# Optimization experiments

Measured on AMD Instinct MI355X. Metric: run time of the kernel, lower is better.

## Reference

```python
import jax, jax.numpy as jnp
import numpy as np

N, E = 50000, 600000
D_IN, D_H, D_OUT = 512, 128, 1
BN_EPS = 1e-5


def setup_inputs() -> dict:
    key = jax.random.key(0)
    ks = jax.random.split(key, 16)
    s = 0.05
    inp = {
        "feature": jax.random.normal(ks[0], (N, D_IN), dtype=jnp.float32),
        "edge_index": jax.random.randint(ks[1], (2, E), 0, N, dtype=jnp.int32),
        "head_W": jax.random.normal(ks[2], (D_IN, D_H), dtype=jnp.float32) * s,
        "head_b": jnp.zeros((D_H,), dtype=jnp.float32),
        "gin_W1": jax.random.normal(ks[3], (D_H, D_H), dtype=jnp.float32) * s,
        "gin_b1": jnp.zeros((D_H,), dtype=jnp.float32),
        "lin_W1": jax.random.normal(ks[4], (D_H, D_H), dtype=jnp.float32) * s,
        "lin_b1": jnp.zeros((D_H,), dtype=jnp.float32),
        "gin_W2": jax.random.normal(ks[5], (D_H, D_H), dtype=jnp.float32) * s,
        "gin_b2": jnp.zeros((D_H,), dtype=jnp.float32),
        "lin_W2": jax.random.normal(ks[6], (D_H, D_H), dtype=jnp.float32) * s,
        "lin_b2": jnp.zeros((D_H,), dtype=jnp.float32),
        "tail_W": jax.random.normal(ks[7], (D_H, D_OUT), dtype=jnp.float32) * s,
        "tail_b": jnp.zeros((D_OUT,), dtype=jnp.float32),
        "bn_gamma": jnp.ones((D_OUT,), dtype=jnp.float32),
        "bn_beta": jnp.zeros((D_OUT,), dtype=jnp.float32),
    }
    return inp


def _gin_layer(x, src, dst, gin_W, gin_b, lin_W, lin_b):
    # PyG GINConv, eps=0: nn((1+eps)*x + sum_{j in N(i)} x_j)
    agg = jax.ops.segment_sum(x[src], dst, num_segments=N)  # [N, D_H]
    h = jax.nn.relu((x + agg) @ gin_W + gin_b)              # GIN MLP (dropout p=0)
    return h @ lin_W + lin_b                                # plain post-linear


def reference(feature, edge_index, head_W, head_b,
              gin_W1, gin_b1, lin_W1, lin_b1,
              gin_W2, gin_b2, lin_W2, lin_b2,
              tail_W, tail_b, bn_gamma, bn_beta):
    src, dst = edge_index[0], edge_index[1]
    x = jax.nn.relu(feature @ head_W + head_b)              # head block (dropout p=0)
    x = _gin_layer(x, src, dst, gin_W1, gin_b1, lin_W1, lin_b1)
    x = _gin_layer(x, src, dst, gin_W2, gin_b2, lin_W2, lin_b2)
    z = x @ tail_W + tail_b                                 # [N, 1]
    # BatchNorm1d in training mode: biased batch stats over the node dim
    mu = jnp.mean(z, axis=0, keepdims=True)
    var = jnp.mean((z - mu) ** 2, axis=0, keepdims=True)
    return (z - mu) * jax.lax.rsqrt(var + BN_EPS) * bn_gamma + bn_beta
```

## Files before the change

### kernel.cpp

```cpp
#include <hip/hip_runtime.h>

#define N_NODES 50000
#define N_EDGES 600000
#define DH 128
#define BN_EPS 1e-5f
#define SCAN_BLOCKS ((N_NODES + 255) / 256)

typedef __attribute__((ext_vector_type(8))) short bf16x8;
typedef __attribute__((ext_vector_type(4))) float f32x4;

__device__ inline unsigned short f2bf(float x) {
  unsigned u = __float_as_uint(x);
  return (unsigned short)((u + 0x7FFFu + ((u >> 16) & 1u)) >> 16);
}
__device__ inline float bf2f(unsigned short h) {
  return __uint_as_float(((unsigned)h) << 16);
}

__device__ inline void gl_lds16(const unsigned short* g, unsigned short* l) {
  __builtin_amdgcn_global_load_lds(
      (const __attribute__((address_space(1))) unsigned int*)g,
      (__attribute__((address_space(3))) unsigned int*)l, 16, 0, 0);
}

__global__ __launch_bounds__(256) void convert_W5_count(
    const float* __restrict__ hW, const float* __restrict__ g1,
    const float* __restrict__ l1, const float* __restrict__ g2,
    const float* __restrict__ l2,
    unsigned short* __restrict__ hH, unsigned short* __restrict__ hL,
    unsigned short* __restrict__ g1H, unsigned short* __restrict__ g1L,
    unsigned short* __restrict__ l1H, unsigned short* __restrict__ l1L,
    unsigned short* __restrict__ g2H, unsigned short* __restrict__ g2L,
    unsigned short* __restrict__ l2H, unsigned short* __restrict__ l2L,
    const int* __restrict__ eidx, int* __restrict__ cnt) {
  int b = blockIdx.x;
  if (b >= 512) {
    int e = (b - 512) * 256 + threadIdx.x;
    if (e < N_EDGES) atomicAdd(&cnt[eidx[N_EDGES + e]], 1);
    return;
  }
  const float* W;
  unsigned short *hi, *lo;
  int idx;
  if (b < 256) {
    W = hW; hi = hH; lo = hL;
    idx = b * 256 + threadIdx.x;
  } else {
    int w = (b - 256) >> 6;
    idx = ((b - 256) & 63) * 256 + threadIdx.x;
    W = (w == 0) ? g1 : (w == 1) ? l1 : (w == 2) ? g2 : l2;
    hi = (w == 0) ? g1H : (w == 1) ? l1H : (w == 2) ? g2H : l2H;
    lo = (w == 0) ? g1L : (w == 1) ? l1L : (w == 2) ? g2L : l2L;
  }
  int k = idx >> 7;
  int n = idx & 127;
  float x = W[idx];
  unsigned short h = f2bf(x);
  unsigned short l = f2bf(x - bf2f(h));
  int kstep = k >> 5;
  int ctile = ((n >> 6) << 2) | (n & 3);
  int cs = (n >> 2) & 15;
  int lane = ((k >> 3) & 3) * 16 + cs;
  int j = k & 7;
  size_t off = ((size_t)(kstep * 8 + ctile) * 64 + lane) * 8 + j;
  hi[off] = h;
  lo[off] = l;
}

__global__ __launch_bounds__(256) void gemm_head(const float* __restrict__ A,
                                                 const unsigned short* __restrict__ Bh,
                                                 const unsigned short* __restrict__ Bl,
                                                 const float* __restrict__ bias,
                                                 float* __restrict__ C,
                                                 unsigned short* __restrict__ xb_out,
                                                 int M) {
  constexpr int K = 512;
  constexpr int KSTEPS = K / 32;
  constexpr int ASTR = 40;
  __shared__ __align__(16) unsigned short Ah[64 * ASTR];
  __shared__ __align__(16) unsigned short Bhs[4096];
  __shared__ __align__(16) unsigned short Bls[4096];

  const int tid = threadIdx.x;
  const int wave = tid >> 6;
  const int lane = tid & 63;
  const int m0 = blockIdx.x * 64;

  const int s_row = tid >> 2;
  const int s_grp = tid & 3;
  const int g_row = m0 + s_row;
  const int g_rowc = (g_row < M) ? g_row : (M - 1);
  const float* af = A + (size_t)g_rowc * K + s_grp * 8;

  const int rgrp = wave & 1;
  const int ch = wave >> 1;

  f32x4 acc[2][4];
#pragma unroll
  for (int r = 0; r < 2; ++r)
#pragma unroll
    for (int c = 0; c < 4; ++c) acc[r][c] = (f32x4){0.f, 0.f, 0.f, 0.f};

  for (int ks = 0; ks < KSTEPS; ++ks) {
    {
      float4 f0 = *(const float4*)(af + ks * 32);
      float4 f1 = *(const float4*)(af + ks * 32 + 4);
      ushort4 h0, h1;
      h0.x = f2bf(f0.x); h0.y = f2bf(f0.y); h0.z = f2bf(f0.z); h0.w = f2bf(f0.w);
      h1.x = f2bf(f1.x); h1.y = f2bf(f1.y); h1.z = f2bf(f1.z); h1.w = f2bf(f1.w);
      int base = s_row * ASTR + s_grp * 8;
      *(ushort4*)&Ah[base + 0] = h0;
      *(ushort4*)&Ah[base + 4] = h1;
    }
    {
      const unsigned short* sh = Bh + (size_t)ks * 4096 + wave * 1024;
      const unsigned short* sl = Bl + (size_t)ks * 4096 + wave * 1024;
      gl_lds16(sh + lane * 8, &Bhs[wave * 1024]);
      gl_lds16(sh + 512 + lane * 8, &Bhs[wave * 1024 + 512]);
      gl_lds16(sl + lane * 8, &Bls[wave * 1024]);
      gl_lds16(sl + 512 + lane * 8, &Bls[wave * 1024 + 512]);
    }
    __syncthreads();

    bf16x8 a0 = *(const bf16x8*)&Ah[(rgrp * 32 + (lane & 15)) * ASTR + (lane >> 4) * 8];
    bf16x8 a1 = *(const bf16x8*)&Ah[(rgrp * 32 + 16 + (lane & 15)) * ASTR + (lane >> 4) * 8];
#pragma unroll
    for (int c = 0; c < 4; ++c) {
      int ct = ch * 4 + c;
      bf16x8 bh = *(const bf16x8*)&Bhs[(ct * 64 + lane) * 8];
      bf16x8 bl = *(const bf16x8*)&Bls[(ct * 64 + lane) * 8];
      acc[0][c] = __builtin_amdgcn_mfma_f32_16x16x32_bf16(a0, bh, acc[0][c], 0, 0, 0);
      acc[0][c] = __builtin_amdgcn_mfma_f32_16x16x32_bf16(a0, bl, acc[0][c], 0, 0, 0);
      acc[1][c] = __builtin_amdgcn_mfma_f32_16x16x32_bf16(a1, bh, acc[1][c], 0, 0, 0);
      acc[1][c] = __builtin_amdgcn_mfma_f32_16x16x32_bf16(a1, bl, acc[1][c], 0, 0, 0);
    }
    __syncthreads();
  }

  const int coln = lane & 15;
  const int rown = (lane >> 4) * 4;
  const int colbase = ch * 64 + coln * 4;
  const float4 bv = *(const float4*)(bias + colbase);
#pragma unroll
  for (int r = 0; r < 2; ++r) {
#pragma unroll
    for (int reg = 0; reg < 4; ++reg) {
      int row = m0 + rgrp * 32 + r * 16 + rown + reg;
      if (row < M) {
        float4 v;
        v.x = fmaxf(acc[r][0][reg] + bv.x, 0.f);
        v.y = fmaxf(acc[r][1][reg] + bv.y, 0.f);
        v.z = fmaxf(acc[r][2][reg] + bv.z, 0.f);
        v.w = fmaxf(acc[r][3][reg] + bv.w, 0.f);
        *(float4*)&C[(size_t)row * DH + colbase] = v;
        ushort4 hb;
        hb.x = f2bf(v.x); hb.y = f2bf(v.y); hb.z = f2bf(v.z); hb.w = f2bf(v.w);
        *(ushort4*)&xb_out[(size_t)row * DH + colbase] = hb;
      }
    }
  }
}

__global__ __launch_bounds__(256) void gemm_gin(
    const unsigned short* __restrict__ yb,
    const unsigned short* __restrict__ B1h, const unsigned short* __restrict__ B1l,
    const float* __restrict__ b1,
    const unsigned short* __restrict__ B2h, const unsigned short* __restrict__ B2l,
    const float* __restrict__ b2, float* __restrict__ X,
    unsigned short* __restrict__ xb_out, int M) {
  constexpr int K = 128;
  constexpr int KSTEPS = K / 32;
  constexpr int ASTR = 40;
  constexpr int HSTR = 136;
  __shared__ __align__(16) unsigned short Ah[64 * ASTR];
  __shared__ __align__(16) unsigned short Bhs[4096];
  __shared__ __align__(16) unsigned short Bls[4096];
  __shared__ __align__(16) unsigned short Hb[64 * HSTR];

  const int tid = threadIdx.x;
  const int wave = tid >> 6;
  const int lane = tid & 63;
  const int m0 = blockIdx.x * 64;

  const int s_row = tid >> 2;
  const int s_oct = tid & 3;
  const int g_row = m0 + s_row;
  const int g_rowc = (g_row < M) ? g_row : (M - 1);
  const unsigned short* ab = yb + (size_t)g_rowc * K + s_oct * 8;

  const int rgrp = wave & 1;
  const int ch = wave >> 1;
  const int coln = lane & 15;
  const int rown = (lane >> 4) * 4;
  const int colbase = ch * 64 + coln * 4;

  auto issueB = [&](const unsigned short* Bh, const unsigned short* Bl, int ks) {
    const unsigned short* sh = Bh + (size_t)ks * 4096 + wave * 1024;
    const unsigned short* sl = Bl + (size_t)ks * 4096 + wave * 1024;
    gl_lds16(sh + lane * 8, &Bhs[wave * 1024]);
    gl_lds16(sh + 512 + lane * 8, &Bhs[wave * 1024 + 512]);
    gl_lds16(sl + lane * 8, &Bls[wave * 1024]);
    gl_lds16(sl + 512 + lane * 8, &Bls[wave * 1024 + 512]);
  };

  f32x4 acc[2][4];
#pragma unroll
  for (int r = 0; r < 2; ++r)
#pragma unroll
    for (int c = 0; c < 4; ++c) acc[r][c] = (f32x4){0.f, 0.f, 0.f, 0.f};

  for (int ks = 0; ks < KSTEPS; ++ks) {
    *(uint4*)&Ah[s_row * ASTR + s_oct * 8] = *(const uint4*)(ab + ks * 32);
    issueB(B1h, B1l, ks);
    __syncthreads();
    bf16x8 a0 = *(const bf16x8*)&Ah[(rgrp * 32 + (lane & 15)) * ASTR + (lane >> 4) * 8];
    bf16x8 a1 = *(const bf16x8*)&Ah[(rgrp * 32 + 16 + (lane & 15)) * ASTR + (lane >> 4) * 8];
#pragma unroll
    for (int c = 0; c < 4; ++c) {
      int ct = ch * 4 + c;
      bf16x8 bh = *(const bf16x8*)&Bhs[(ct * 64 + lane) * 8];
      bf16x8 bl = *(const bf16x8*)&Bls[(ct * 64 + lane) * 8];
      acc[0][c] = __builtin_amdgcn_mfma_f32_16x16x32_bf16(a0, bh, acc[0][c], 0, 0, 0);
      acc[0][c] = __builtin_amdgcn_mfma_f32_16x16x32_bf16(a0, bl, acc[0][c], 0, 0, 0);
      acc[1][c] = __builtin_amdgcn_mfma_f32_16x16x32_bf16(a1, bh, acc[1][c], 0, 0, 0);
      acc[1][c] = __builtin_amdgcn_mfma_f32_16x16x32_bf16(a1, bl, acc[1][c], 0, 0, 0);
    }
    __syncthreads();
  }

  {
    const float4 bv = *(const float4*)(b1 + colbase);
#pragma unroll
    for (int r = 0; r < 2; ++r) {
#pragma unroll
      for (int reg = 0; reg < 4; ++reg) {
        int lrow = rgrp * 32 + r * 16 + rown + reg;
        ushort4 hb;
        hb.x = f2bf(fmaxf(acc[r][0][reg] + bv.x, 0.f));
        hb.y = f2bf(fmaxf(acc[r][1][reg] + bv.y, 0.f));
        hb.z = f2bf(fmaxf(acc[r][2][reg] + bv.z, 0.f));
        hb.w = f2bf(fmaxf(acc[r][3][reg] + bv.w, 0.f));
        *(ushort4*)&Hb[lrow * HSTR + colbase] = hb;
      }
    }
#pragma unroll
    for (int r = 0; r < 2; ++r)
#pragma unroll
      for (int c = 0; c < 4; ++c) acc[r][c] = (f32x4){0.f, 0.f, 0.f, 0.f};
  }

  for (int ks = 0; ks < KSTEPS; ++ks) {
    issueB(B2h, B2l, ks);
    __syncthreads();
    bf16x8 a0 = *(const bf16x8*)&Hb[(rgrp * 32 + (lane & 15)) * HSTR + ks * 32 + (lane >> 4) * 8];
    bf16x8 a1 = *(const bf16x8*)&Hb[(rgrp * 32 + 16 + (lane & 15)) * HSTR + ks * 32 + (lane >> 4) * 8];
#pragma unroll
    for (int c = 0; c < 4; ++c) {
      int ct = ch * 4 + c;
      bf16x8 bh = *(const bf16x8*)&Bhs[(ct * 64 + lane) * 8];
      bf16x8 bl = *(const bf16x8*)&Bls[(ct * 64 + lane) * 8];
      acc[0][c] = __builtin_amdgcn_mfma_f32_16x16x32_bf16(a0, bh, acc[0][c], 0, 0, 0);
      acc[0][c] = __builtin_amdgcn_mfma_f32_16x16x32_bf16(a0, bl, acc[0][c], 0, 0, 0);
      acc[1][c] = __builtin_amdgcn_mfma_f32_16x16x32_bf16(a1, bh, acc[1][c], 0, 0, 0);
      acc[1][c] = __builtin_amdgcn_mfma_f32_16x16x32_bf16(a1, bl, acc[1][c], 0, 0, 0);
    }
    __syncthreads();
  }

  {
    const float4 bv = *(const float4*)(b2 + colbase);
#pragma unroll
    for (int r = 0; r < 2; ++r) {
#pragma unroll
      for (int reg = 0; reg < 4; ++reg) {
        int row = m0 + rgrp * 32 + r * 16 + rown + reg;
        if (row < M) {
          float4 v;
          v.x = acc[r][0][reg] + bv.x;
          v.y = acc[r][1][reg] + bv.y;
          v.z = acc[r][2][reg] + bv.z;
          v.w = acc[r][3][reg] + bv.w;
          *(float4*)&X[(size_t)row * DH + colbase] = v;
          if (xb_out) {
            ushort4 hb;
            hb.x = f2bf(v.x); hb.y = f2bf(v.y); hb.z = f2bf(v.z); hb.w = f2bf(v.w);
            *(ushort4*)&xb_out[(size_t)row * DH + colbase] = hb;
          }
        }
      }
    }
  }
}

__global__ __launch_bounds__(256) void scan_block(const int* __restrict__ cnt,
                                                  int* __restrict__ rs,
                                                  int* __restrict__ partials) {
  int t = threadIdx.x;
  int i = blockIdx.x * 256 + t;
  int v = (i < N_NODES) ? cnt[i] : 0;
  __shared__ int s[256];
  s[t] = v;
  __syncthreads();
#pragma unroll
  for (int off = 1; off < 256; off <<= 1) {
    int add = (t >= off) ? s[t - off] : 0;
    __syncthreads();
    s[t] += add;
    __syncthreads();
  }
  if (i < N_NODES) rs[i] = s[t] - v;
  if (t == 255) partials[blockIdx.x] = s[255];
}

__global__ __launch_bounds__(256) void scan_partials(int* __restrict__ partials) {
  int t = threadIdx.x;
  int v = (t < SCAN_BLOCKS) ? partials[t] : 0;
  __shared__ int s[256];
  s[t] = v;
  __syncthreads();
#pragma unroll
  for (int off = 1; off < 256; off <<= 1) {
    int add = (t >= off) ? s[t - off] : 0;
    __syncthreads();
    s[t] += add;
    __syncthreads();
  }
  if (t < SCAN_BLOCKS) partials[t] = s[t] - v;
}

__global__ __launch_bounds__(256) void add_offsets(int* __restrict__ rs,
                                                   const int* __restrict__ partials) {
  int i = blockIdx.x * 256 + threadIdx.x;
  if (i < N_NODES) rs[i] += partials[blockIdx.x];
  if (i == 0) rs[N_NODES] = N_EDGES;
}

__global__ __launch_bounds__(256) void fill_csr(const int* __restrict__ eidx,
                                                const int* __restrict__ rs,
                                                int* __restrict__ cursor,
                                                int* __restrict__ esrc) {
  int e = blockIdx.x * 256 + threadIdx.x;
  if (e >= N_EDGES) return;
  int d = eidx[N_EDGES + e];
  int p = atomicAdd(&cursor[d], 1);
  esrc[rs[d] + p] = eidx[e];
}

__global__ __launch_bounds__(256) void gin_aggregate_bf16(
    const unsigned short* __restrict__ xb, const float* __restrict__ x,
    const int* __restrict__ rs, const int* __restrict__ esrc,
    unsigned* __restrict__ yb) {
  int node = blockIdx.x * 4 + (threadIdx.x >> 6);
  int lane = threadIdx.x & 63;
  if (node >= N_NODES) return;
  float2 acc = ((const float2*)x)[(size_t)node * 64 + lane];
  const unsigned* xb2 = (const unsigned*)xb;
  int beg = rs[node];
  int end = rs[node + 1];
  int j = beg;
  for (; j + 8 <= end; j += 8) {
    int s0 = esrc[j + 0];
    int s1 = esrc[j + 1];
    int s2 = esrc[j + 2];
    int s3 = esrc[j + 3];
    int s4 = esrc[j + 4];
    int s5 = esrc[j + 5];
    int s6 = esrc[j + 6];
    int s7 = esrc[j + 7];
    unsigned v0 = xb2[(size_t)s0 * 64 + lane];
    unsigned v1 = xb2[(size_t)s1 * 64 + lane];
    unsigned v2 = xb2[(size_t)s2 * 64 + lane];
    unsigned v3 = xb2[(size_t)s3 * 64 + lane];
    unsigned v4 = xb2[(size_t)s4 * 64 + lane];
    unsigned v5 = xb2[(size_t)s5 * 64 + lane];
    unsigned v6 = xb2[(size_t)s6 * 64 + lane];
    unsigned v7 = xb2[(size_t)s7 * 64 + lane];
    acc.x += ((__uint_as_float(v0 << 16) + __uint_as_float(v1 << 16)) +
              (__uint_as_float(v2 << 16) + __uint_as_float(v3 << 16))) +
             ((__uint_as_float(v4 << 16) + __uint_as_float(v5 << 16)) +
              (__uint_as_float(v6 << 16) + __uint_as_float(v7 << 16)));
    acc.y += ((__uint_as_float(v0 & 0xFFFF0000u) + __uint_as_float(v1 & 0xFFFF0000u)) +
              (__uint_as_float(v2 & 0xFFFF0000u) + __uint_as_float(v3 & 0xFFFF0000u))) +
             ((__uint_as_float(v4 & 0xFFFF0000u) + __uint_as_float(v5 & 0xFFFF0000u)) +
              (__uint_as_float(v6 & 0xFFFF0000u) + __uint_as_float(v7 & 0xFFFF0000u)));
  }
  for (; j + 4 <= end; j += 4) {
    int s0 = esrc[j + 0];
    int s1 = esrc[j + 1];
    int s2 = esrc[j + 2];
    int s3 = esrc[j + 3];
    unsigned v0 = xb2[(size_t)s0 * 64 + lane];
    unsigned v1 = xb2[(size_t)s1 * 64 + lane];
    unsigned v2 = xb2[(size_t)s2 * 64 + lane];
    unsigned v3 = xb2[(size_t)s3 * 64 + lane];
    acc.x += (__uint_as_float(v0 << 16) + __uint_as_float(v1 << 16)) +
             (__uint_as_float(v2 << 16) + __uint_as_float(v3 << 16));
    acc.y += (__uint_as_float(v0 & 0xFFFF0000u) + __uint_as_float(v1 & 0xFFFF0000u)) +
             (__uint_as_float(v2 & 0xFFFF0000u) + __uint_as_float(v3 & 0xFFFF0000u));
  }
  for (; j < end; ++j) {
    unsigned v = xb2[(size_t)esrc[j] * 64 + lane];
    acc.x += __uint_as_float(v << 16);
    acc.y += __uint_as_float(v & 0xFFFF0000u);
  }
  yb[(size_t)node * 64 + lane] =
      (unsigned)f2bf(acc.x) | ((unsigned)f2bf(acc.y) << 16);
}

__global__ __launch_bounds__(256) void tail_bn1(const float* __restrict__ x,
                                                const float* __restrict__ tw,
                                                const float* __restrict__ tb,
                                                float* __restrict__ z,
                                                float* __restrict__ red) {
  const int lane = threadIdx.x & 31;
  const int grp = threadIdx.x >> 5;
  float4 w = *(const float4*)(tw + lane * 4);
  float accS = 0.f, accQ = 0.f;
  for (int node = blockIdx.x * 8 + grp; node < N_NODES; node += gridDim.x * 8) {
    float4 v = *(const float4*)(x + (size_t)node * DH + lane * 4);
    float p = v.x * w.x + v.y * w.y + v.z * w.z + v.w * w.w;
#pragma unroll
    for (int m = 16; m; m >>= 1) p += __shfl_xor(p, m, 32);
    if (lane == 0) {
      float zv = p + tb[0];
      z[node] = zv;
      accS += zv;
      accQ += zv * zv;
    }
  }
  __shared__ float sS[256];
  __shared__ float sQ[256];
  sS[threadIdx.x] = accS;
  sQ[threadIdx.x] = accQ;
  __syncthreads();
  for (int s = 128; s; s >>= 1) {
    if (threadIdx.x < s) {
      sS[threadIdx.x] += sS[threadIdx.x + s];
      sQ[threadIdx.x] += sQ[threadIdx.x + s];
    }
    __syncthreads();
  }
  if (threadIdx.x == 0) {
    atomicAdd(&red[0], sS[0]);
    atomicAdd(&red[1], sQ[0]);
  }
}

__global__ __launch_bounds__(256) void bn2(const float* __restrict__ z,
                                           const float* __restrict__ red,
                                           const float* __restrict__ gamma,
                                           const float* __restrict__ beta,
                                           float* __restrict__ out) {
  int i = blockIdx.x * 256 + threadIdx.x;
  if (i >= N_NODES) return;
  float mu = red[0] * (1.0f / N_NODES);
  float var = red[1] * (1.0f / N_NODES) - mu * mu;
  out[i] = (z[i] - mu) * rsqrtf(var + BN_EPS) * gamma[0] + beta[0];
}

extern "C" void kernel_launch(void* const* d_in, const int* in_sizes, int n_in,
                              void* d_out, int out_size, void* d_ws, size_t ws_size,
                              hipStream_t stream) {
  const float* feature = (const float*)d_in[0];
  const int* eidx = (const int*)d_in[1];
  const float* head_W = (const float*)d_in[2];
  const float* head_b = (const float*)d_in[3];
  const float* gin_W1 = (const float*)d_in[4];
  const float* gin_b1 = (const float*)d_in[5];
  const float* lin_W1 = (const float*)d_in[6];
  const float* lin_b1 = (const float*)d_in[7];
  const float* gin_W2 = (const float*)d_in[8];
  const float* gin_b2 = (const float*)d_in[9];
  const float* lin_W2 = (const float*)d_in[10];
  const float* lin_b2 = (const float*)d_in[11];
  const float* tail_W = (const float*)d_in[12];
  const float* tail_b = (const float*)d_in[13];
  const float* bn_gamma = (const float*)d_in[14];
  const float* bn_beta = (const float*)d_in[15];

  float* X = (float*)d_ws;
  float* z = X + (size_t)N_NODES * DH;
  float* red = z + N_NODES;
  int* row_start = (int*)(red + 2);
  int* cnt = row_start + (N_NODES + 1);
  int* partials = cnt + N_NODES;
  int* esrc = partials + 256;
  unsigned short* wp =
      (unsigned short*)(((uintptr_t)(esrc + N_EDGES) + 15) & ~(uintptr_t)15);
  unsigned short* hH = wp;
  unsigned short* hL = hH + 65536;
  unsigned short* g1H = hL + 65536;
  unsigned short* g1L = g1H + 16384;
  unsigned short* l1H = g1L + 16384;
  unsigned short* l1L = l1H + 16384;
  unsigned short* g2H = l1L + 16384;
  unsigned short* g2L = g2H + 16384;
  unsigned short* l2H = g2L + 16384;
  unsigned short* l2L = l2H + 16384;
  unsigned short* xb = l2L + 16384;
  unsigned short* yb = xb + (size_t)N_NODES * DH;

  const int head_grid = (N_NODES + 63) / 64;
  const int gemm_grid = (N_NODES + 63) / 64;
  const int edge_grid = (N_EDGES + 255) / 256;
  const int agg_grid = (N_NODES + 3) / 4;

  hipMemsetAsync(cnt, 0, N_NODES * sizeof(int), stream);
  hipMemsetAsync(red, 0, 2 * sizeof(float), stream);

  convert_W5_count<<<512 + edge_grid, 256, 0, stream>>>(
      head_W, gin_W1, lin_W1, gin_W2, lin_W2, hH, hL, g1H, g1L, l1H, l1L,
      g2H, g2L, l2H, l2L, eidx, cnt);

  scan_block<<<SCAN_BLOCKS, 256, 0, stream>>>(cnt, row_start, partials);
  scan_partials<<<1, 256, 0, stream>>>(partials);
  add_offsets<<<SCAN_BLOCKS, 256, 0, stream>>>(row_start, partials);
  hipMemsetAsync(cnt, 0, N_NODES * sizeof(int), stream);
  fill_csr<<<edge_grid, 256, 0, stream>>>(eidx, row_start, cnt, esrc);

  gemm_head<<<head_grid, 256, 0, stream>>>(feature, hH, hL, head_b, X, xb,
                                           N_NODES);

  gin_aggregate_bf16<<<agg_grid, 256, 0, stream>>>(xb, X, row_start, esrc,
                                                   (unsigned*)yb);
  gemm_gin<<<gemm_grid, 256, 0, stream>>>(yb, g1H, g1L, gin_b1, l1H, l1L,
                                          lin_b1, X, xb, N_NODES);

  gin_aggregate_bf16<<<agg_grid, 256, 0, stream>>>(xb, X, row_start, esrc,
                                                   (unsigned*)yb);
  gemm_gin<<<gemm_grid, 256, 0, stream>>>(yb, g2H, g2L, gin_b2, l2H, l2L,
                                          lin_b2, X, nullptr, N_NODES);

  tail_bn1<<<256, 256, 0, stream>>>(X, tail_W, tail_b, z, red);
  bn2<<<(N_NODES + 255) / 256, 256, 0, stream>>>(z, red, bn_gamma, bn_beta, (float*)d_out);
}
```

Measured before the change: 400.9 us.

## Pipeline head GEMM with register-direct A loads and double-buffered B

Reworks the head GEMM to load A rows straight from global into registers, converting to bf16 in-register, so the LDS staging of A and its barrier are gone. The B tiles are double-buffered in LDS and A loads are prefetched two steps ahead using a triple register buffer with explicit waitcnt, which overlaps memory with MFMA. The block tile drops from 64 to 32 rows, doubling the grid. In exchange each B tile is fetched twice as often per row, and the correctness of the hand-written vmcnt counting becomes fragile.

```diff
diff --git a/kernel.cpp b/kernel.cpp
--- a/kernel.cpp
+++ b/kernel.cpp
@@ -76,65 +76,80 @@
                                                  int M) {
   constexpr int K = 512;
   constexpr int KSTEPS = K / 32;
-  constexpr int ASTR = 40;
-  __shared__ __align__(16) unsigned short Ah[64 * ASTR];
-  __shared__ __align__(16) unsigned short Bhs[4096];
-  __shared__ __align__(16) unsigned short Bls[4096];
+  __shared__ __align__(16) unsigned short Bhs[2][4096];
+  __shared__ __align__(16) unsigned short Bls[2][4096];
 
   const int tid = threadIdx.x;
   const int wave = tid >> 6;
   const int lane = tid & 63;
-  const int m0 = blockIdx.x * 64;
-
-  const int s_row = tid >> 2;
-  const int s_grp = tid & 3;
-  const int g_row = m0 + s_row;
-  const int g_rowc = (g_row < M) ? g_row : (M - 1);
-  const float* af = A + (size_t)g_rowc * K + s_grp * 8;
-
-  const int rgrp = wave & 1;
+  const int m0 = blockIdx.x * 32;
+
+  const int rh = wave & 1;
   const int ch = wave >> 1;
 
-  f32x4 acc[2][4];
-#pragma unroll
-  for (int r = 0; r < 2; ++r)
-#pragma unroll
-    for (int c = 0; c < 4; ++c) acc[r][c] = (f32x4){0.f, 0.f, 0.f, 0.f};
-
+  int arow = m0 + rh * 16 + (lane & 15);
+  if (arow >= M) arow = M - 1;
+  const float* aptr = A + (size_t)arow * K + (lane >> 4) * 8;
+
+  auto issueB = [&](int ks, int buf) {
+    const unsigned short* sh = Bh + (size_t)ks * 4096 + wave * 1024;
+    const unsigned short* sl = Bl + (size_t)ks * 4096 + wave * 1024;
+    gl_lds16(sh + lane * 8, &Bhs[buf][wave * 1024]);
+    gl_lds16(sh + 512 + lane * 8, &Bhs[buf][wave * 1024 + 512]);
+    gl_lds16(sl + lane * 8, &Bls[buf][wave * 1024]);
+    gl_lds16(sl + 512 + lane * 8, &Bls[buf][wave * 1024 + 512]);
+  };
+
+  auto loadA = [&](f32x4& lo4, f32x4& hi4, const float* ap) {
+    asm volatile("global_load_dwordx4 %0, %1, off"
+                 : "=&v"(lo4) : "v"(ap) : "memory");
+    asm volatile("global_load_dwordx4 %0, %1, off offset:16"
+                 : "=&v"(hi4) : "v"(ap) : "memory");
+  };
+
+  f32x4 acc[4];
+#pragma unroll
+  for (int c = 0; c < 4; ++c) acc[c] = (f32x4){0.f, 0.f, 0.f, 0.f};
+
+  f32x4 alo[3], ahi[3];
+
+  loadA(alo[0], ahi[0], aptr);
+  issueB(0, 0);
+  loadA(alo[1], ahi[1], aptr + 32);
+
+#pragma unroll
   for (int ks = 0; ks < KSTEPS; ++ks) {
-    {
-      float4 f0 = *(const float4*)(af + ks * 32);
-      float4 f1 = *(const float4*)(af + ks * 32 + 4);
-      ushort4 h0, h1;
-      h0.x = f2bf(f0.x); h0.y = f2bf(f0.y); h0.z = f2bf(f0.z); h0.w = f2bf(f0.w);
-      h1.x = f2bf(f1.x); h1.y = f2bf(f1.y); h1.z = f2bf(f1.z); h1.w = f2bf(f1.w);
-      int base = s_row * ASTR + s_grp * 8;
-      *(ushort4*)&Ah[base + 0] = h0;
-      *(ushort4*)&Ah[base + 4] = h1;
-    }
-    {
-      const unsigned short* sh = Bh + (size_t)ks * 4096 + wave * 1024;
-      const unsigned short* sl = Bl + (size_t)ks * 4096 + wave * 1024;
-      gl_lds16(sh + lane * 8, &Bhs[wave * 1024]);
-      gl_lds16(sh + 512 + lane * 8, &Bhs[wave * 1024 + 512]);
-      gl_lds16(sl + lane * 8, &Bls[wave * 1024]);
-      gl_lds16(sl + 512 + lane * 8, &Bls[wave * 1024 + 512]);
-    }
-    __syncthreads();
-
-    bf16x8 a0 = *(const bf16x8*)&Ah[(rgrp * 32 + (lane & 15)) * ASTR + (lane >> 4) * 8];
-    bf16x8 a1 = *(const bf16x8*)&Ah[(rgrp * 32 + 16 + (lane & 15)) * ASTR + (lane >> 4) * 8];
+    const int cur = ks & 1;
+    const int s = ks % 3;
+    if (ks < KSTEPS - 1)
+      asm volatile("s_waitcnt vmcnt(2)"
+                   : "+v"(alo[s]), "+v"(ahi[s]) :: "memory");
+    else
+      asm volatile("s_waitcnt vmcnt(0)"
+                   : "+v"(alo[s]), "+v"(ahi[s]) :: "memory");
+    __builtin_amdgcn_s_barrier();
+    __builtin_amdgcn_sched_barrier(0);
+
+    if (ks + 1 < KSTEPS) issueB(ks + 1, cur ^ 1);
+    if (ks + 2 < KSTEPS) {
+      const int s2 = (ks + 2) % 3;
+      loadA(alo[s2], ahi[s2], aptr + (ks + 2) * 32);
+    }
+
+    bf16x8 a0;
+    a0[0] = (short)f2bf(alo[s][0]); a0[1] = (short)f2bf(alo[s][1]);
+    a0[2] = (short)f2bf(alo[s][2]); a0[3] = (short)f2bf(alo[s][3]);
+    a0[4] = (short)f2bf(ahi[s][0]); a0[5] = (short)f2bf(ahi[s][1]);
+    a0[6] = (short)f2bf(ahi[s][2]); a0[7] = (short)f2bf(ahi[s][3]);
+
 #pragma unroll
     for (int c = 0; c < 4; ++c) {
       int ct = ch * 4 + c;
-      bf16x8 bh = *(const bf16x8*)&Bhs[(ct * 64 + lane) * 8];
-      bf16x8 bl = *(const bf16x8*)&Bls[(ct * 64 + lane) * 8];
-      acc[0][c] = __builtin_amdgcn_mfma_f32_16x16x32_bf16(a0, bh, acc[0][c], 0, 0, 0);
-      acc[0][c] = __builtin_amdgcn_mfma_f32_16x16x32_bf16(a0, bl, acc[0][c], 0, 0, 0);
-      acc[1][c] = __builtin_amdgcn_mfma_f32_16x16x32_bf16(a1, bh, acc[1][c], 0, 0, 0);
-      acc[1][c] = __builtin_amdgcn_mfma_f32_16x16x32_bf16(a1, bl, acc[1][c], 0, 0, 0);
-    }
-    __syncthreads();
+      bf16x8 bh = *(const bf16x8*)&Bhs[cur][(ct * 64 + lane) * 8];
+      bf16x8 bl = *(const bf16x8*)&Bls[cur][(ct * 64 + lane) * 8];
+      acc[c] = __builtin_amdgcn_mfma_f32_16x16x32_bf16(a0, bh, acc[c], 0, 0, 0);
+      acc[c] = __builtin_amdgcn_mfma_f32_16x16x32_bf16(a0, bl, acc[c], 0, 0, 0);
+    }
   }
 
   const int coln = lane & 15;
@@ -142,21 +157,18 @@
   const int colbase = ch * 64 + coln * 4;
   const float4 bv = *(const float4*)(bias + colbase);
 #pragma unroll
-  for (int r = 0; r < 2; ++r) {
-#pragma unroll
-    for (int reg = 0; reg < 4; ++reg) {
-      int row = m0 + rgrp * 32 + r * 16 + rown + reg;
-      if (row < M) {
-        float4 v;
-        v.x = fmaxf(acc[r][0][reg] + bv.x, 0.f);
-        v.y = fmaxf(acc[r][1][reg] + bv.y, 0.f);
-        v.z = fmaxf(acc[r][2][reg] + bv.z, 0.f);
-        v.w = fmaxf(acc[r][3][reg] + bv.w, 0.f);
-        *(float4*)&C[(size_t)row * DH + colbase] = v;
-        ushort4 hb;
-        hb.x = f2bf(v.x); hb.y = f2bf(v.y); hb.z = f2bf(v.z); hb.w = f2bf(v.w);
-        *(ushort4*)&xb_out[(size_t)row * DH + colbase] = hb;
-      }
+  for (int reg = 0; reg < 4; ++reg) {
+    int row = m0 + rh * 16 + rown + reg;
+    if (row < M) {
+      float4 v;
+      v.x = fmaxf(acc[0][reg] + bv.x, 0.f);
+      v.y = fmaxf(acc[1][reg] + bv.y, 0.f);
+      v.z = fmaxf(acc[2][reg] + bv.z, 0.f);
+      v.w = fmaxf(acc[3][reg] + bv.w, 0.f);
+      *(float4*)&C[(size_t)row * DH + colbase] = v;
+      ushort4 hb;
+      hb.x = f2bf(v.x); hb.y = f2bf(v.y); hb.z = f2bf(v.z); hb.w = f2bf(v.w);
+      *(ushort4*)&xb_out[(size_t)row * DH + colbase] = hb;
     }
   }
 }
@@ -500,8 +512,8 @@
   unsigned short* xb = l2L + 16384;
   unsigned short* yb = xb + (size_t)N_NODES * DH;
 
-  const int head_grid = (N_NODES + 63) / 64;
-  const int gemm_grid = (N_NODES + 63) / 64;
+  const int head_grid = (N_NODES + 31) / 32;
+  const int gin_grid = (N_NODES + 63) / 64;
   const int edge_grid = (N_EDGES + 255) / 256;
   const int agg_grid = (N_NODES + 3) / 4;
 
@@ -523,13 +535,13 @@
 
   gin_aggregate_bf16<<<agg_grid, 256, 0, stream>>>(xb, X, row_start, esrc,
                                                    (unsigned*)yb);
-  gemm_gin<<<gemm_grid, 256, 0, stream>>>(yb, g1H, g1L, gin_b1, l1H, l1L,
-                                          lin_b1, X, xb, N_NODES);
+  gemm_gin<<<gin_grid, 256, 0, stream>>>(yb, g1H, g1L, gin_b1, l1H, l1L,
+                                         lin_b1, X, xb, N_NODES);
 
   gin_aggregate_bf16<<<agg_grid, 256, 0, stream>>>(xb, X, row_start, esrc,
                                                    (unsigned*)yb);
-  gemm_gin<<<gemm_grid, 256, 0, stream>>>(yb, g2H, g2L, gin_b2, l2H, l2L,
-                                          lin_b2, X, nullptr, N_NODES);
+  gemm_gin<<<gin_grid, 256, 0, stream>>>(yb, g2H, g2L, gin_b2, l2H, l2L,
+                                         lin_b2, X, nullptr, N_NODES);
 
   tail_bn1<<<256, 256, 0, stream>>>(X, tail_W, tail_b, z, red);
   bn2<<<(N_NODES + 255) / 256, 256, 0, stream>>>(z, red, bn_gamma, bn_beta, (float*)d_out);
```

Measured after the change: 413.0 us. 3.0% more time.
